# Performance work log

Hardware: AMD Instinct MI355X
Metric: run time of the kernel (lower is better)

## Reference

```python
import jax, jax.numpy as jnp
import numpy as np

BUCKET_SIZE = 64  # init kwarg bucket_size
DIM = 64          # init kwarg dim (per-head dim, used for scaling)


def setup_inputs() -> dict:
    key = jax.random.key(0)
    kq, kk = jax.random.split(key)
    q = jax.random.normal(kq, (32, 8192, 64), dtype=jnp.float32)
    k = jax.random.normal(kk, (32, 8192, 64), dtype=jnp.float32)
    return {"q": q, "k": k}


def _cumavg(t):
    # cumulative average along the sequence axis (axis=1)
    r = jnp.arange(1, t.shape[1] + 1, dtype=t.dtype)
    return jnp.cumsum(t, axis=1) / r[None, :, None]


def reference(q, k):
    bh, n, d = q.shape
    buckets = n // BUCKET_SIZE
    kv_buckets = k.shape[1] // BUCKET_SIZE

    # bucket the cumulative averages: [bh, buckets, bucket_size, d]
    q_r = _cumavg(q).reshape(bh, buckets, BUCKET_SIZE, d)
    k_r = _cumavg(k).reshape(bh, kv_buckets, BUCKET_SIZE, d)

    sq = q_r[:, :, 0]                                   # [bh, buckets, d]
    sk = k_r.sum(axis=2)                                # [bh, kv_buckets, d]
    sk = jnp.pad(sk, ((0, 0), (1, 0), (0, 0)))          # pad one zero bucket row at front

    R = jnp.einsum('bie,bje->bij', sq, sk) * (DIM ** -0.5)  # [bh, buckets, kv_buckets+1]

    rows = jnp.arange(buckets)[:, None]
    cols = jnp.arange(kv_buckets + 1)[None, :]
    neg = -jnp.finfo(R.dtype).max
    # masked_fill: for row i, columns i+1..buckets set to -max (cols > rows)
    R = jnp.where(cols > rows, neg, R)
    R = jax.nn.softmax(R, axis=-1)
    # tril(diagonal=-1): keep entries with col < row
    R = jnp.where(cols < rows, R, jnp.zeros((), R.dtype))
    return R
```

## Files before the change

### kernel.cpp

```cpp
#include <hip/hip_runtime.h>
#include <cstddef>

constexpr int BH = 32;
constexpr int N  = 8192;
constexpr int D  = 64;
constexpr int BK = 64;
constexpr int NB = 128;
constexpr int NC = 129;

__global__ __launch_bounds__(256) void kA(const float* __restrict__ q,
                                          const float* __restrict__ k,
                                          float* __restrict__ qsum,
                                          float* __restrict__ ksum,
                                          float* __restrict__ kw,
                                          float* __restrict__ qfirst,
                                          float* __restrict__ W) {
  const int j   = blockIdx.x;
  const int b   = blockIdx.y;
  const int tid = threadIdx.x;
  const int base = j * BK;

  __shared__ float winv[BK];
  __shared__ float tailw[BK];
  __shared__ float red[3][16][D];

  if (tid < BK) winv[tid] = 1.0f / (float)(base + tid + 1);
  __syncthreads();
  if (tid < BK) {
    float s = 0.0f;
    for (int u = BK - 1; u >= tid; --u) s += winv[u];
    tailw[tid] = s;
  }
  __syncthreads();

  const float4* q4 = (const float4*)(q + ((size_t)b * N + base) * D);
  const float4* k4 = (const float4*)(k + ((size_t)b * N + base) * D);
  const int f  = tid & 15;
  const int r0 = tid >> 4;

  float aq[4] = {0,0,0,0}, ak[4] = {0,0,0,0}, aw[4] = {0,0,0,0};
  float qf[4] = {0,0,0,0};

#pragma unroll
  for (int p = 0; p < 4; ++p) {
    const int row = p * 16 + r0;
    const float4 qv = q4[row * 16 + f];
    const float4 kv = k4[row * 16 + f];
    const float tw = tailw[row];
    aq[0] += qv.x; aq[1] += qv.y; aq[2] += qv.z; aq[3] += qv.w;
    ak[0] += kv.x; ak[1] += kv.y; ak[2] += kv.z; ak[3] += kv.w;
    aw[0] += kv.x * tw; aw[1] += kv.y * tw; aw[2] += kv.z * tw; aw[3] += kv.w * tw;
    if (p == 0 && r0 == 0) { qf[0] = qv.x; qf[1] = qv.y; qf[2] = qv.z; qf[3] = qv.w; }
  }

#pragma unroll
  for (int c = 0; c < 4; ++c) {
    red[0][r0][4*f + c] = aq[c];
    red[1][r0][4*f + c] = ak[c];
    red[2][r0][4*f + c] = aw[c];
  }
  __syncthreads();

  const size_t ob = ((size_t)b * NB + j) * D;
  if (tid < D) {
    float sq_ = 0.f, sk_ = 0.f, sw_ = 0.f;
#pragma unroll
    for (int r = 0; r < 16; ++r) {
      sq_ += red[0][r][tid];
      sk_ += red[1][r][tid];
      sw_ += red[2][r][tid];
    }
    qsum[ob + tid] = sq_;
    ksum[ob + tid] = sk_;
    kw[ob + tid]   = sw_;
  }
  if (r0 == 0) {
    ((float4*)(qfirst + ob))[f] = make_float4(qf[0], qf[1], qf[2], qf[3]);
  }
  if (tid == 0 && b == 0) W[j] = tailw[0];
}

__global__ __launch_bounds__(256) void kB(const float* __restrict__ qsum,
                                          const float* __restrict__ ksum,
                                          const float* __restrict__ kw,
                                          const float* __restrict__ qfirst,
                                          const float* __restrict__ W,
                                          float* __restrict__ sq,
                                          float* __restrict__ skp) {
  const int b   = blockIdx.x;
  const int tid = threadIdx.x;
  const int d   = tid & 63;
  const int jg  = tid >> 6;

  __shared__ float qtot[4][D], ktot[4][D];

  const float* qs = qsum + (size_t)b * NB * D;
  const float* ks = ksum + (size_t)b * NB * D;

  float qt = 0.f, kt = 0.f;
  for (int jj = 0; jj < 32; ++jj) {
    const int j = jg * 32 + jj;
    qt += qs[j * D + d];
    kt += ks[j * D + d];
  }
  qtot[jg][d] = qt;
  ktot[jg][d] = kt;
  __syncthreads();

  float qpre = 0.f, kpre = 0.f;
  for (int g = 0; g < jg; ++g) { qpre += qtot[g][d]; kpre += ktot[g][d]; }

  if (tid < D) skp[(size_t)b * NC * D + tid] = 0.0f;

  for (int jj = 0; jj < 32; ++jj) {
    const int j = jg * 32 + jj;
    const size_t o = ((size_t)b * NB + j) * D + d;
    sq[o] = (qpre + qfirst[o]) / (float)(j * BK + 1);
    skp[((size_t)b * NC + j + 1) * D + d] = kpre * W[j] + kw[o];
    qpre += qs[j * D + d];
    kpre += ks[j * D + d];
  }
}

__global__ __launch_bounds__(256) void kC(const float* __restrict__ sq,
                                          const float* __restrict__ skp,
                                          float* __restrict__ out) {
  const int i   = blockIdx.x;
  const int b   = blockIdx.y;
  const int tid = threadIdx.x;

  __shared__ float srow[D];
  __shared__ float rbuf[256];

  if (tid < D) srow[tid] = sq[((size_t)b * NB + i) * D + tid];
  __syncthreads();

  const bool valid = (tid <= i);
  float dot = 0.0f;
  if (valid) {
    const float4* kr = (const float4*)(skp + ((size_t)b * NC + tid) * D);
    const float4* sr = (const float4*)srow;
#pragma unroll
    for (int f = 0; f < 16; ++f) {
      const float4 a = sr[f];
      const float4 c = kr[f];
      dot += a.x * c.x + a.y * c.y + a.z * c.z + a.w * c.w;
    }
    dot *= 0.125f;
  }

  rbuf[tid] = valid ? dot : -3.402823466e38f;
  __syncthreads();
  for (int s = 128; s > 0; s >>= 1) {
    if (tid < s) rbuf[tid] = fmaxf(rbuf[tid], rbuf[tid + s]);
    __syncthreads();
  }
  const float mx = rbuf[0];
  __syncthreads();

  const float e = valid ? expf(dot - mx) : 0.0f;
  rbuf[tid] = e;
  __syncthreads();
  for (int s = 128; s > 0; s >>= 1) {
    if (tid < s) rbuf[tid] += rbuf[tid + s];
    __syncthreads();
  }
  const float denom = rbuf[0];

  if (tid < NC) {
    out[((size_t)b * NB + i) * NC + tid] = (tid < i) ? (e / denom) : 0.0f;
  }
}

extern "C" void kernel_launch(void* const* d_in, const int* in_sizes, int n_in,
                              void* d_out, int out_size, void* d_ws, size_t ws_size,
                              hipStream_t stream) {
  const float* q = (const float*)d_in[0];
  const float* k = (const float*)d_in[1];
  float* out = (float*)d_out;

  float* ws     = (float*)d_ws;
  float* qsum   = ws;
  float* ksum   = qsum   + (size_t)BH * NB * D;
  float* kw     = ksum   + (size_t)BH * NB * D;
  float* qfirst = kw     + (size_t)BH * NB * D;
  float* sq     = qfirst + (size_t)BH * NB * D;
  float* skp    = sq     + (size_t)BH * NB * D;
  float* W      = skp    + (size_t)BH * NC * D;

  kA<<<dim3(NB, BH), 256, 0, stream>>>(q, k, qsum, ksum, kw, qfirst, W);
  kB<<<dim3(BH), 256, 0, stream>>>(qsum, ksum, kw, qfirst, W, sq, skp);
  kC<<<dim3(NB, BH), 256, 0, stream>>>(sq, skp, out);
}
```

Baseline: 170.2 us.

## Use wave-level reductions in all three kernels and split scan kernel across q/k

kA now assigns one 64-row bucket per wavefront instead of one per block. It computes the tail weights inline and reduces with cross-lane shuffles instead of shared memory and barriers. kB launches two blocks per head, one for the q prefix and one for the k prefix, and stages the bucket sums in LDS to double parallelism in the serial scan stage. kC shrinks to 128 threads and replaces the tree reductions in shared memory with wave shuffles plus a two-entry combine. The aim is to cut barrier and LDS overhead and the low occupancy of kB, at the cost of more register and shuffle work and a slightly different floating-point summation order.

Measured after the change: 176.2 us. 3.5% more time.

```diff
diff --git a/kernel.cpp b/kernel.cpp
--- a/kernel.cpp
+++ b/kernel.cpp
@@ -15,69 +15,61 @@
                                           float* __restrict__ kw,
                                           float* __restrict__ qfirst,
                                           float* __restrict__ W) {
-  const int j   = blockIdx.x;
-  const int b   = blockIdx.y;
-  const int tid = threadIdx.x;
+  const int tid  = threadIdx.x;
+  const int wv   = tid >> 6;
+  const int lane = tid & 63;
+  const int f    = lane & 15;
+  const int r0   = lane >> 4;
+  const int j    = blockIdx.x * 4 + wv;
+  const int b    = blockIdx.y;
   const int base = j * BK;
-
-  __shared__ float winv[BK];
-  __shared__ float tailw[BK];
-  __shared__ float red[3][16][D];
-
-  if (tid < BK) winv[tid] = 1.0f / (float)(base + tid + 1);
-  __syncthreads();
-  if (tid < BK) {
-    float s = 0.0f;
-    for (int u = BK - 1; u >= tid; --u) s += winv[u];
-    tailw[tid] = s;
-  }
-  __syncthreads();
 
   const float4* q4 = (const float4*)(q + ((size_t)b * N + base) * D);
   const float4* k4 = (const float4*)(k + ((size_t)b * N + base) * D);
-  const int f  = tid & 15;
-  const int r0 = tid >> 4;
 
   float aq[4] = {0,0,0,0}, ak[4] = {0,0,0,0}, aw[4] = {0,0,0,0};
   float qf[4] = {0,0,0,0};
+  float wh = 0.0f;
 
 #pragma unroll
-  for (int p = 0; p < 4; ++p) {
-    const int row = p * 16 + r0;
+  for (int t = 15; t >= 0; --t) {
+    const int row = (r0 << 4) + t;
+    wh += 1.0f / (float)(base + row + 1);
     const float4 qv = q4[row * 16 + f];
     const float4 kv = k4[row * 16 + f];
-    const float tw = tailw[row];
     aq[0] += qv.x; aq[1] += qv.y; aq[2] += qv.z; aq[3] += qv.w;
     ak[0] += kv.x; ak[1] += kv.y; ak[2] += kv.z; ak[3] += kv.w;
-    aw[0] += kv.x * tw; aw[1] += kv.y * tw; aw[2] += kv.z * tw; aw[3] += kv.w * tw;
-    if (p == 0 && r0 == 0) { qf[0] = qv.x; qf[1] = qv.y; qf[2] = qv.z; qf[3] = qv.w; }
+    aw[0] += kv.x * wh; aw[1] += kv.y * wh; aw[2] += kv.z * wh; aw[3] += kv.w * wh;
+    if (t == 0 && r0 == 0) { qf[0] = qv.x; qf[1] = qv.y; qf[2] = qv.z; qf[3] = qv.w; }
   }
+
+  const float w16 = __shfl_xor(wh, 16);
+  const float w32 = __shfl_xor(wh, 32);
+  const float w48 = __shfl_xor(wh, 48);
+  float TU = 0.0f;
+  if ((r0 ^ 1) > r0) TU += w16;
+  if ((r0 ^ 2) > r0) TU += w32;
+  if ((r0 ^ 3) > r0) TU += w48;
+  const float Wfull = wh + w16 + w32 + w48;
+
+#pragma unroll
+  for (int c = 0; c < 4; ++c) aw[c] += TU * ak[c];
 
 #pragma unroll
   for (int c = 0; c < 4; ++c) {
-    red[0][r0][4*f + c] = aq[c];
-    red[1][r0][4*f + c] = ak[c];
-    red[2][r0][4*f + c] = aw[c];
+    aq[c] += __shfl_xor(aq[c], 16); aq[c] += __shfl_xor(aq[c], 32);
+    ak[c] += __shfl_xor(ak[c], 16); ak[c] += __shfl_xor(ak[c], 32);
+    aw[c] += __shfl_xor(aw[c], 16); aw[c] += __shfl_xor(aw[c], 32);
   }
-  __syncthreads();
 
-  const size_t ob = ((size_t)b * NB + j) * D;
-  if (tid < D) {
-    float sq_ = 0.f, sk_ = 0.f, sw_ = 0.f;
-#pragma unroll
-    for (int r = 0; r < 16; ++r) {
-      sq_ += red[0][r][tid];
-      sk_ += red[1][r][tid];
-      sw_ += red[2][r][tid];
-    }
-    qsum[ob + tid] = sq_;
-    ksum[ob + tid] = sk_;
-    kw[ob + tid]   = sw_;
+  if (r0 == 0) {
+    const size_t ob = ((size_t)b * NB + j) * D;
+    ((float4*)(qsum   + ob))[f] = make_float4(aq[0], aq[1], aq[2], aq[3]);
+    ((float4*)(ksum   + ob))[f] = make_float4(ak[0], ak[1], ak[2], ak[3]);
+    ((float4*)(kw     + ob))[f] = make_float4(aw[0], aw[1], aw[2], aw[3]);
+    ((float4*)(qfirst + ob))[f] = make_float4(qf[0], qf[1], qf[2], qf[3]);
+    if (f == 0 && b == 0) W[j] = Wfull;
   }
-  if (r0 == 0) {
-    ((float4*)(qfirst + ob))[f] = make_float4(qf[0], qf[1], qf[2], qf[3]);
-  }
-  if (tid == 0 && b == 0) W[j] = tailw[0];
 }
 
 __global__ __launch_bounds__(256) void kB(const float* __restrict__ qsum,
@@ -87,58 +79,71 @@
                                           const float* __restrict__ W,
                                           float* __restrict__ sq,
                                           float* __restrict__ skp) {
-  const int b   = blockIdx.x;
-  const int tid = threadIdx.x;
-  const int d   = tid & 63;
-  const int jg  = tid >> 6;
+  const int side = blockIdx.x;
+  const int b    = blockIdx.y;
+  const int tid  = threadIdx.x;
+  const int d    = tid & 63;
+  const int jg   = tid >> 6;
 
-  __shared__ float qtot[4][D], ktot[4][D];
+  __shared__ float buf[NB * D];
+  __shared__ float tot[4 * D];
+  __shared__ float Wl[NB];
 
-  const float* qs = qsum + (size_t)b * NB * D;
-  const float* ks = ksum + (size_t)b * NB * D;
-
-  float qt = 0.f, kt = 0.f;
-  for (int jj = 0; jj < 32; ++jj) {
-    const int j = jg * 32 + jj;
-    qt += qs[j * D + d];
-    kt += ks[j * D + d];
+  const float* src = (side == 0 ? qsum : ksum) + (size_t)b * NB * D;
+  {
+    const float4* g4 = (const float4*)src;
+    float4* l4 = (float4*)buf;
+    for (int u = tid; u < NB * D / 4; u += 256) l4[u] = g4[u];
+    if (side == 1 && tid < NB) Wl[tid] = W[tid];
   }
-  qtot[jg][d] = qt;
-  ktot[jg][d] = kt;
   __syncthreads();
 
-  float qpre = 0.f, kpre = 0.f;
-  for (int g = 0; g < jg; ++g) { qpre += qtot[g][d]; kpre += ktot[g][d]; }
+  float t0 = 0.0f;
+  for (int jj = 0; jj < 32; ++jj) t0 += buf[(jg * 32 + jj) * D + d];
+  tot[jg * D + d] = t0;
+  __syncthreads();
 
-  if (tid < D) skp[(size_t)b * NC * D + tid] = 0.0f;
+  float pre = 0.0f;
+  for (int g = 0; g < jg; ++g) pre += tot[g * D + d];
 
-  for (int jj = 0; jj < 32; ++jj) {
-    const int j = jg * 32 + jj;
-    const size_t o = ((size_t)b * NB + j) * D + d;
-    sq[o] = (qpre + qfirst[o]) / (float)(j * BK + 1);
-    skp[((size_t)b * NC + j + 1) * D + d] = kpre * W[j] + kw[o];
-    qpre += qs[j * D + d];
-    kpre += ks[j * D + d];
+  if (side == 0) {
+    for (int jj = 0; jj < 32; ++jj) {
+      const int j = jg * 32 + jj;
+      const size_t o = ((size_t)b * NB + j) * D + d;
+      sq[o] = (pre + qfirst[o]) / (float)(j * BK + 1);
+      pre += buf[j * D + d];
+    }
+  } else {
+    if (tid < D) skp[(size_t)b * NC * D + tid] = 0.0f;
+    for (int jj = 0; jj < 32; ++jj) {
+      const int j = jg * 32 + jj;
+      const size_t o = ((size_t)b * NB + j) * D + d;
+      skp[((size_t)b * NC + j + 1) * D + d] = pre * Wl[j] + kw[o];
+      pre += buf[j * D + d];
+    }
   }
 }
 
-__global__ __launch_bounds__(256) void kC(const float* __restrict__ sq,
+__global__ __launch_bounds__(128) void kC(const float* __restrict__ sq,
                                           const float* __restrict__ skp,
                                           float* __restrict__ out) {
   const int i   = blockIdx.x;
   const int b   = blockIdx.y;
   const int tid = threadIdx.x;
+  const int wv  = tid >> 6;
 
   __shared__ float srow[D];
-  __shared__ float rbuf[256];
+  __shared__ float wred[2][2];
 
-  if (tid < D) srow[tid] = sq[((size_t)b * NB + i) * D + tid];
+  if (tid < 16)
+    ((float4*)srow)[tid] = ((const float4*)(sq + ((size_t)b * NB + i) * D))[tid];
   __syncthreads();
 
-  const bool valid = (tid <= i);
+  const int j = tid;
+  const bool valid = (j <= i);
   float dot = 0.0f;
   if (valid) {
-    const float4* kr = (const float4*)(skp + ((size_t)b * NC + tid) * D);
+    const float4* kr = (const float4*)(skp + ((size_t)b * NC + j) * D);
     const float4* sr = (const float4*)srow;
 #pragma unroll
     for (int f = 0; f < 16; ++f) {
@@ -149,27 +154,24 @@
     dot *= 0.125f;
   }
 
-  rbuf[tid] = valid ? dot : -3.402823466e38f;
+  float m = valid ? dot : -3.402823466e38f;
+#pragma unroll
+  for (int s = 32; s; s >>= 1) m = fmaxf(m, __shfl_xor(m, s));
+  if ((tid & 63) == 0) wred[0][wv] = m;
   __syncthreads();
-  for (int s = 128; s > 0; s >>= 1) {
-    if (tid < s) rbuf[tid] = fmaxf(rbuf[tid], rbuf[tid + s]);
-    __syncthreads();
-  }
-  const float mx = rbuf[0];
-  __syncthreads();
+  const float mx = fmaxf(wred[0][0], wred[0][1]);
 
   const float e = valid ? expf(dot - mx) : 0.0f;
-  rbuf[tid] = e;
+  float ss = e;
+#pragma unroll
+  for (int s = 32; s; s >>= 1) ss += __shfl_xor(ss, s);
+  if ((tid & 63) == 0) wred[1][wv] = ss;
   __syncthreads();
-  for (int s = 128; s > 0; s >>= 1) {
-    if (tid < s) rbuf[tid] += rbuf[tid + s];
-    __syncthreads();
-  }
-  const float denom = rbuf[0];
+  const float denom = wred[1][0] + wred[1][1];
 
-  if (tid < NC) {
-    out[((size_t)b * NB + i) * NC + tid] = (tid < i) ? (e / denom) : 0.0f;
-  }
+  float* orow = out + ((size_t)b * NB + i) * NC;
+  orow[j] = (j < i) ? (e / denom) : 0.0f;
+  if (tid == 0) orow[128] = 0.0f;
 }
 
 extern "C" void kernel_launch(void* const* d_in, const int* in_sizes, int n_in,
@@ -188,7 +190,7 @@
   float* skp    = sq     + (size_t)BH * NB * D;
   float* W      = skp    + (size_t)BH * NC * D;
 
-  kA<<<dim3(NB, BH), 256, 0, stream>>>(q, k, qsum, ksum, kw, qfirst, W);
-  kB<<<dim3(BH), 256, 0, stream>>>(qsum, ksum, kw, qfirst, W, sq, skp);
-  kC<<<dim3(NB, BH), 256, 0, stream>>>(sq, skp, out);
+  kA<<<dim3(NB / 4, BH), 256, 0, stream>>>(q, k, qsum, ksum, kw, qfirst, W);
+  kB<<<dim3(2, BH), 256, 0, stream>>>(qsum, ksum, kw, qfirst, W, sq, skp);
+  kC<<<dim3(NB, BH), 128, 0, stream>>>(sq, skp, out);
 }
```
